# Kernel tuning notes

Measured on AMD Instinct MI355X. Metric: run time of the kernel, lower is better.

Reference implementation:

```python
import jax, jax.numpy as jnp
import numpy as np

N_NODES = 100000
N_EDGES = 1600000
N_GRAPHS = 2048
HID = 64
IN_F = 14
N_CLS = 2
EPS = 1e-5


def _gcn_conv(x, row, col, w_edge, W, b, n_nodes):
    # PyG GCNConv with add_self_loops=True, normalize=True.
    xw = x @ W  # [N, out]
    # degree on target nodes, self-loop contributes weight 1
    deg = jnp.zeros((n_nodes,), x.dtype).at[col].add(w_edge) + 1.0
    dinv = deg ** -0.5
    norm = dinv[row] * w_edge * dinv[col]  # [E]
    out = jnp.zeros_like(xw).at[col].add(norm[:, None] * xw[row])
    out = out + (dinv * dinv)[:, None] * xw  # self-loop term
    return out + b


def _bn_relu(x, gamma, beta):
    mean = jnp.mean(x, axis=0)
    var = jnp.var(x, axis=0)  # biased, as PyTorch BN training normalization
    y = gamma * (x - mean) * jax.lax.rsqrt(var + EPS) + beta
    return jax.nn.relu(y)


def setup_inputs() -> dict:
    key = jax.random.key(0)
    ks = jax.random.split(key, 8)
    x = jax.random.normal(ks[0], (N_NODES, IN_F), dtype=jnp.float32)
    edge_index = jax.random.randint(ks[1], (2, N_EDGES), 0, N_NODES, dtype=jnp.int64)
    batch = jnp.sort(jax.random.randint(ks[2], (N_NODES,), 0, N_GRAPHS, dtype=jnp.int64))
    edge_weight = jnp.ones((N_EDGES,), dtype=jnp.float32)
    def lin(k, fi, fo):
        s = 1.0 / np.sqrt(fi)
        kw, kb = jax.random.split(k)
        return (jax.random.uniform(kw, (fi, fo), jnp.float32, -s, s),
                jax.random.uniform(kb, (fo,), jnp.float32, -s, s))
    W1, b1 = lin(ks[3], IN_F, HID)
    W2, b2 = lin(ks[4], HID, HID)
    W3, b3 = lin(ks[5], HID, HID)
    fcW, fcb = lin(ks[6], HID, N_CLS)
    g = jnp.ones((HID,), jnp.float32)
    z = jnp.zeros((HID,), jnp.float32)
    return {
        "x": x, "edge_index": edge_index, "batch": batch, "edge_weight": edge_weight,
        "W1": W1, "b1": b1, "W2": W2, "b2": b2, "W3": W3, "b3": b3,
        "g1": g, "bt1": z, "g2": g, "bt2": z, "g3": g, "bt3": z,
        "fcW": fcW, "fcb": fcb,
    }


def reference(x, edge_index, batch, edge_weight, W1, b1, W2, b2, W3, b3,
              g1, bt1, g2, bt2, g3, bt3, fcW, fcb):
    row, col = edge_index[0], edge_index[1]
    n = x.shape[0]
    h = _bn_relu(_gcn_conv(x, row, col, edge_weight, W1, b1, n), g1, bt1)
    h = _bn_relu(_gcn_conv(h, row, col, edge_weight, W2, b2, n), g2, bt2)
    h = _bn_relu(_gcn_conv(h, row, col, edge_weight, W3, b3, n), g3, bt3)
    node_embs = h  # dropout p=0 is identity
    graph_emb = jax.ops.segment_sum(node_embs, batch, num_segments=N_GRAPHS)
    out = graph_emb @ fcW + fcb
    return (out, node_embs, graph_emb)
```

## Files before the change

kernel.cpp:

```cpp
#include <hip/hip_runtime.h>
#include <hip/hip_fp16.h>

#define N_NODES 100000
#define N_EDGES 1600000
#define EMAX2   1700000
#define N_GRAPHS 2048
#define HID 64
#define IN_F 14
#define N_CLS 2
#define EPS 1e-5f

#define BSHIFT 9
#define NBUCK 196
#define ABLOCKS 256
#define CHUNK (N_EDGES / ABLOCKS)

#define NBLK2 128
#define NCHUNK2 ((N_NODES + NBLK2 - 1) / NBLK2)

typedef _Float16 half_t;
typedef _Float16 half8 __attribute__((ext_vector_type(8)));
typedef float f32x4 __attribute__((ext_vector_type(4)));

#define GSTRIDE ((size_t)N_NODES * 16)


__global__ __launch_bounds__(256) void histA_kernel(const int* __restrict__ col,
                                                    int* __restrict__ histG) {
    __shared__ int hl[NBUCK];
    for (int i = threadIdx.x; i < NBUCK; i += 256) hl[i] = 0;
    __syncthreads();
    int e0 = blockIdx.x * CHUNK;
    for (int e = e0 + threadIdx.x; e < e0 + CHUNK; e += 256)
        atomicAdd(&hl[col[e] >> BSHIFT], 1);
    __syncthreads();
    for (int i = threadIdx.x; i < NBUCK; i += 256)
        histG[i * ABLOCKS + blockIdx.x] = hl[i];
}

__global__ __launch_bounds__(256) void scanS1_kernel(const int* __restrict__ histG,
                                                     int* __restrict__ bsumA) {
    __shared__ int ls[256];
    ls[threadIdx.x] = histG[blockIdx.x * 256 + threadIdx.x];
    __syncthreads();
    for (int off = 128; off > 0; off >>= 1) {
        if (threadIdx.x < off) ls[threadIdx.x] += ls[threadIdx.x + off];
        __syncthreads();
    }
    if (threadIdx.x == 0) bsumA[blockIdx.x] = ls[0];
}

__global__ __launch_bounds__(512) void topscan_kernel(int* __restrict__ bsum, int nb) {
    __shared__ int ls[512];
    int t = threadIdx.x;
    int v = (t < nb) ? bsum[t] : 0;
    ls[t] = v;
    __syncthreads();
    for (int off = 1; off < 512; off <<= 1) {
        int x = ls[t];
        if (t >= off) x += ls[t - off];
        __syncthreads();
        ls[t] = x;
        __syncthreads();
    }
    if (t < nb) bsum[t] = ls[t] - v;
}

__global__ __launch_bounds__(256) void scanS3_kernel(int* __restrict__ histG,
                                                     const int* __restrict__ bsumA,
                                                     int* __restrict__ ptr) {
    __shared__ int ls[256];
    int idx = blockIdx.x * 256 + threadIdx.x;
    int v = histG[idx];
    ls[threadIdx.x] = v;
    __syncthreads();
    for (int off = 1; off < 256; off <<= 1) {
        int x = ls[threadIdx.x];
        if (threadIdx.x >= off) x += ls[threadIdx.x - off];
        __syncthreads();
        ls[threadIdx.x] = x;
        __syncthreads();
    }
    histG[idx] = ls[threadIdx.x] - v + bsumA[blockIdx.x];
    if (blockIdx.x == 0 && threadIdx.x == 0) ptr[N_NODES] = N_EDGES;
}

__global__ __launch_bounds__(256) void scatterA_kernel(const int* __restrict__ row,
                                                       const int* __restrict__ col,
                                                       const float* __restrict__ w,
                                                       const int* __restrict__ histG,
                                                       int2* __restrict__ EA) {
    __shared__ int cur[NBUCK];
    for (int i = threadIdx.x; i < NBUCK; i += 256)
        cur[i] = histG[i * ABLOCKS + blockIdx.x];
    __syncthreads();
    int e0 = blockIdx.x * CHUNK;
    for (int e = e0 + threadIdx.x; e < e0 + CHUNK; e += 256) {
        int c = col[e];
        int r = row[e];
        int fx = (int)__float2uint_rn(w[e] * 8192.0f);
        int pos = atomicAdd(&cur[c >> BSHIFT], 1);
        EA[pos] = make_int2(r, (fx << 17) | c);
    }
}

__global__ __launch_bounds__(256) void bucketA_kernel(const int2* __restrict__ EA,
                                                      const int* __restrict__ bsumA,
                                                      int* __restrict__ ptr,
                                                      float* __restrict__ dinv) {
    __shared__ int hist[512], wsum[512];
    int b = blockIdx.x;
    int beg = bsumA[b];
    int end = (b == NBUCK - 1) ? N_EDGES : bsumA[b + 1];
    int i0 = threadIdx.x, i1 = threadIdx.x + 256;
    hist[i0] = 0; hist[i1] = 0;
    wsum[i0] = 0; wsum[i1] = 0;
    __syncthreads();
    for (int e = beg + threadIdx.x; e < end; e += 256) {
        int2 ed = EA[e];
        int c9 = ed.y & 511;
        atomicAdd(&hist[c9], 1);
        atomicAdd(&wsum[c9], (int)((unsigned int)ed.y >> 17));
    }
    __syncthreads();
    int cnt0 = hist[i0], cnt1 = hist[i1];
    for (int off = 1; off < 512; off <<= 1) {
        int v0 = hist[i0], v1 = hist[i1];
        int a0 = (i0 >= off) ? hist[i0 - off] : 0;
        int a1 = (i1 >= off) ? hist[i1 - off] : 0;
        __syncthreads();
        hist[i0] = v0 + a0;
        hist[i1] = v1 + a1;
        __syncthreads();
    }
    int excl0 = hist[i0] - cnt0, excl1 = hist[i1] - cnt1;
    int col0 = (b << BSHIFT) + i0, col1 = (b << BSHIFT) + i1;
    if (col0 < N_NODES) {
        ptr[col0] = beg + excl0;
        dinv[col0] = rsqrtf(1.0f + (float)wsum[i0] * (1.0f / 8192.0f));
    }
    if (col1 < N_NODES) {
        ptr[col1] = beg + excl1;
        dinv[col1] = rsqrtf(1.0f + (float)wsum[i1] * (1.0f / 8192.0f));
    }
}


__global__ __launch_bounds__(256) void histD_kernel(const int* __restrict__ ptr,
                                                    int* __restrict__ histD) {
    __shared__ int hl[2048];
    for (int i = threadIdx.x; i < 2048; i += 256) hl[i] = 0;
    __syncthreads();
    int n0 = blockIdx.x * NCHUNK2;
    int n1 = n0 + NCHUNK2; if (n1 > N_NODES) n1 = N_NODES;
    for (int n = n0 + threadIdx.x; n < n1; n += 256) {
        int d = ptr[n + 1] - ptr[n];
        if (d > 255) d = 255;
        atomicAdd(&hl[((threadIdx.x & 7) << 8) + d], 1);
    }
    __syncthreads();
    int s = 0;
#pragma unroll
    for (int c = 0; c < 8; c++) s += hl[(c << 8) + threadIdx.x];
    histD[threadIdx.x * NBLK2 + blockIdx.x] = s;
}

__global__ __launch_bounds__(128) void scanD1_kernel(const int* __restrict__ histD,
                                                     int* __restrict__ rowTot) {
    __shared__ int ls[128];
    ls[threadIdx.x] = histD[blockIdx.x * NBLK2 + threadIdx.x];
    __syncthreads();
    for (int off = 64; off > 0; off >>= 1) {
        if (threadIdx.x < off) ls[threadIdx.x] += ls[threadIdx.x + off];
        __syncthreads();
    }
    if (threadIdx.x == 0) rowTot[blockIdx.x] = ls[0];
}

__global__ __launch_bounds__(256) void topscanD_kernel(const int* __restrict__ rowTot,
                                                       int* __restrict__ nodeExcl,
                                                       int* __restrict__ edgeExcl,
                                                       int* __restrict__ ptrS) {
    __shared__ int a[256], b[256];
    int t = threadIdx.x;
    int cnt = rowTot[t];
    int dpad = (t + 1) & ~1;
    int ec = cnt * dpad;
    a[t] = cnt; b[t] = ec;
    __syncthreads();
    for (int off = 1; off < 256; off <<= 1) {
        int va = a[t], vb = b[t];
        if (t >= off) { va += a[t - off]; vb += b[t - off]; }
        __syncthreads();
        a[t] = va; b[t] = vb;
        __syncthreads();
    }
    nodeExcl[t] = a[t] - cnt;
    edgeExcl[t] = b[t] - ec;
    if (t == 255) ptrS[N_NODES] = b[255];
}

__global__ __launch_bounds__(128) void scanD3_kernel(int* __restrict__ histD,
                                                     const int* __restrict__ nodeExcl) {
    __shared__ int ls[128];
    int idx = blockIdx.x * NBLK2 + threadIdx.x;
    int v = histD[idx];
    ls[threadIdx.x] = v;
    __syncthreads();
    for (int off = 1; off < 128; off <<= 1) {
        int x = ls[threadIdx.x];
        if (threadIdx.x >= off) x += ls[threadIdx.x - off];
        __syncthreads();
        ls[threadIdx.x] = x;
        __syncthreads();
    }
    histD[idx] = ls[threadIdx.x] - v + nodeExcl[blockIdx.x];
}

__global__ __launch_bounds__(256) void scatterD_kernel(const int* __restrict__ ptr,
                                                       const int* __restrict__ histD,
                                                       const int* __restrict__ nodeExcl,
                                                       const int* __restrict__ edgeExcl,
                                                       int* __restrict__ perm,
                                                       int* __restrict__ ptrS,
                                                       int* __restrict__ newbase) {
    __shared__ int cur[256];
    cur[threadIdx.x] = histD[threadIdx.x * NBLK2 + blockIdx.x];
    __syncthreads();
    int n0 = blockIdx.x * NCHUNK2;
    int n1 = n0 + NCHUNK2; if (n1 > N_NODES) n1 = N_NODES;
    for (int n = n0 + threadIdx.x; n < n1; n += 256) {
        int d = ptr[n + 1] - ptr[n];
        if (d > 255) d = 255;
        int dpad = (d + 1) & ~1;
        int pos = atomicAdd(&cur[d], 1);
        int ebase = edgeExcl[d] + (pos - nodeExcl[d]) * dpad;
        perm[pos] = n;
        ptrS[pos] = ebase;
        newbase[n] = ebase;
    }
}

__global__ __launch_bounds__(256) void bucketB_kernel(const int2* __restrict__ EA,
                                                      const int* __restrict__ bsumA,
                                                      const int* __restrict__ newbase,
                                                      const float* __restrict__ dinv,
                                                      unsigned int* __restrict__ srcoff,
                                                      half_t* __restrict__ normh) {
    __shared__ int cur[512];
    int b = blockIdx.x;
    int beg = bsumA[b];
    int end = (b == NBUCK - 1) ? N_EDGES : bsumA[b + 1];
    int i0 = threadIdx.x, i1 = threadIdx.x + 256;
    int col0 = (b << BSHIFT) + i0, col1 = (b << BSHIFT) + i1;
    cur[i0] = (col0 < N_NODES) ? newbase[col0] : 0;
    cur[i1] = (col1 < N_NODES) ? newbase[col1] : 0;
    __syncthreads();
    for (int e = beg + threadIdx.x; e < end; e += 256) {
        int2 ed = EA[e];
        int c = ed.y & 0x1ffff;
        float w = (float)((unsigned int)ed.y >> 17) * (1.0f / 8192.0f);
        float nrm = dinv[ed.x] * w * dinv[c];
        int pos = atomicAdd(&cur[c & 511], 1);
        srcoff[pos] = (unsigned int)ed.x << 5;
        normh[pos] = (half_t)nrm;
    }
}


template <int K>
__global__ __launch_bounds__(256) void gemm_kernel(const float* __restrict__ h,
                                                   const float* __restrict__ W,
                                                   half_t* __restrict__ xw, int n_nodes) {
    int f = threadIdx.x & 63;
    float wcol[K];
#pragma unroll
    for (int k = 0; k < K; k++) wcol[k] = W[k * HID + f];
    half_t* xg = xw + (size_t)(f >> 4) * GSTRIDE + (f & 15);
    int wave = (blockIdx.x * blockDim.x + threadIdx.x) >> 6;
    int nwaves = (gridDim.x * blockDim.x) >> 6;
    for (int n = wave; n < n_nodes; n += nwaves) {
        const float* hr = h + (size_t)n * K;
        float acc = 0.f;
#pragma unroll
        for (int k = 0; k < K; k++) acc += hr[k] * wcol[k];
        xg[(size_t)n * 16] = (half_t)acc;
    }
}

__global__ __launch_bounds__(256) void gemm_bn_mfma_kernel(const half_t* __restrict__ h,
                                                           const float* __restrict__ W,
                                                           const float* __restrict__ stats,
                                                           const float* __restrict__ gamma,
                                                           const float* __restrict__ beta,
                                                           half_t* __restrict__ xw, int n_nodes) {
    __shared__ float sc_s[HID], sh_s[HID];
    if (threadIdx.x < 64) {
        float mean = stats[threadIdx.x] * (1.0f / N_NODES);
        float var = stats[64 + threadIdx.x] * (1.0f / N_NODES) - mean * mean;
        float sc = gamma[threadIdx.x] * rsqrtf(var + EPS);
        sc_s[threadIdx.x] = sc;
        sh_s[threadIdx.x] = beta[threadIdx.x] - mean * sc;
    }
    __syncthreads();
    int lane = threadIdx.x & 63;
    int col16 = lane & 15;
    int quad = lane >> 4;

    float scA[2][8], shA[2][8];
#pragma unroll
    for (int kh = 0; kh < 2; kh++)
#pragma unroll
        for (int j = 0; j < 8; j++) {
            int k = kh * 32 + quad * 8 + j;
            scA[kh][j] = sc_s[k];
            shA[kh][j] = sh_s[k];
        }

    half8 bfrag[4][2];
#pragma unroll
    for (int t = 0; t < 4; t++)
#pragma unroll
        for (int kh = 0; kh < 2; kh++)
#pragma unroll
            for (int j = 0; j < 8; j++) {
                int k = kh * 32 + quad * 8 + j;
                bfrag[t][kh][j] = (half_t)W[k * HID + t * 16 + col16];
            }

    int wave = (blockIdx.x * blockDim.x + threadIdx.x) >> 6;
    int nwaves = (gridDim.x * blockDim.x) >> 6;
    int ntiles = n_nodes >> 4;
    for (int tIdx = wave; tIdx < ntiles; tIdx += nwaves) {
        int n0 = tIdx << 4;
        half8 afrag[2];
#pragma unroll
        for (int kh = 0; kh < 2; kh++) {
            int k0 = kh * 32 + quad * 8;
            const half_t* hp = h + (size_t)(k0 >> 4) * GSTRIDE
                                 + (size_t)(n0 + col16) * 16 + (k0 & 15);
            half8 raw = *(const half8*)hp;
#pragma unroll
            for (int j = 0; j < 8; j++) {
                float v = (float)raw[j] * scA[kh][j] + shA[kh][j];
                afrag[kh][j] = (half_t)fmaxf(v, 0.f);
            }
        }
        f32x4 acc[4];
#pragma unroll
        for (int t = 0; t < 4; t++) {
            f32x4 z = {0.f, 0.f, 0.f, 0.f};
            acc[t] = __builtin_amdgcn_mfma_f32_16x16x32_f16(afrag[0], bfrag[t][0], z, 0, 0, 0);
            acc[t] = __builtin_amdgcn_mfma_f32_16x16x32_f16(afrag[1], bfrag[t][1], acc[t], 0, 0, 0);
        }
#pragma unroll
        for (int t = 0; t < 4; t++) {
            half_t* xg = xw + (size_t)t * GSTRIDE;
#pragma unroll
            for (int r = 0; r < 4; r++) {
                int rowi = n0 + quad * 4 + r;
                xg[(size_t)rowi * 16 + col16] = (half_t)acc[t][r];
            }
        }
    }
}

__global__ __launch_bounds__(256) void gather_stats_kernel(const int* __restrict__ ptrS,
                                                           const int* __restrict__ perm,
                                                           const unsigned int* __restrict__ srcoff,
                                                           const unsigned int* __restrict__ normu,
                                                           const half_t* __restrict__ xw,
                                                           const float* __restrict__ dinv,
                                                           const float* __restrict__ b,
                                                           half_t* __restrict__ hp,
                                                           float* __restrict__ stats,
                                                           int n_nodes) {
    int g = (blockIdx.x & 7) >> 1;
    int grank = ((blockIdx.x >> 3) << 1) | (blockIdx.x & 1);
    int lane16 = threadIdx.x & 15;
    int quadLocal = threadIdx.x >> 4;
    int quadId = grank * 16 + quadLocal;
    int nquads = (gridDim.x >> 2) * 16;

    const half_t* xg = xw + (size_t)g * GSTRIDE;
    const char* xgc = (const char*)xg;
    unsigned int loff = (unsigned int)(lane16 * 2);
    half_t* hpg = hp + (size_t)g * GSTRIDE;
    int f = g * 16 + lane16;
    float bf = b[f];
    int base = ((threadIdx.x & 63) >> 4) * 16;

    float s = 0.f, s2 = 0.f;
    for (int i = quadId; i < n_nodes; i += nquads) {
        int node = perm[i];
        int beg = ptrS[i];
        int c = ptrS[i + 1] - beg;
        __half2 acc0 = __float2half2_rn(0.f);
        __half2 acc1 = __float2half2_rn(0.f);
        for (int j0 = 0; j0 < c; j0 += 16) {
            int m = c - j0;
            if (m > 16) m = 16;
            int pairs = m >> 1;
            int ev = 0, nv = 0;
            if (lane16 < m) ev = (int)srcoff[beg + j0 + lane16];
            if (lane16 < pairs) nv = (int)normu[((beg + j0) >> 1) + lane16];
            int p = 0;
            for (; p + 2 <= pairs; p += 2) {
                unsigned int u0 = (unsigned int)__shfl(ev, base + 2 * p);
                unsigned int u1 = (unsigned int)__shfl(ev, base + 2 * p + 1);
                unsigned int u2 = (unsigned int)__shfl(ev, base + 2 * p + 2);
                unsigned int u3 = (unsigned int)__shfl(ev, base + 2 * p + 3);
                unsigned int nd0 = (unsigned int)__shfl(nv, base + p);
                unsigned int nd1 = (unsigned int)__shfl(nv, base + p + 1);
                __half h0 = *(const __half*)(xgc + (u0 + loff));
                __half h1 = *(const __half*)(xgc + (u1 + loff));
                __half h2 = *(const __half*)(xgc + (u2 + loff));
                __half h3 = *(const __half*)(xgc + (u3 + loff));
                __half2 n01 = *(__half2*)&nd0;
                __half2 n23 = *(__half2*)&nd1;
                acc0 = __hfma2(n01, __halves2half2(h0, h1), acc0);
                acc1 = __hfma2(n23, __halves2half2(h2, h3), acc1);
            }
            if (p < pairs) {
                unsigned int u0 = (unsigned int)__shfl(ev, base + 2 * p);
                unsigned int u1 = (unsigned int)__shfl(ev, base + 2 * p + 1);
                unsigned int nd0 = (unsigned int)__shfl(nv, base + p);
                __half h0 = *(const __half*)(xgc + (u0 + loff));
                __half h1 = *(const __half*)(xgc + (u1 + loff));
                __half2 n01 = *(__half2*)&nd0;
                acc0 = __hfma2(n01, __halves2half2(h0, h1), acc0);
            }
        }
        float accf = (__low2float(acc0) + __high2float(acc0))
                   + (__low2float(acc1) + __high2float(acc1));
        float di = dinv[node];
        float v = accf + di * di * (float)xg[(size_t)node * 16 + lane16] + bf;
        hpg[(size_t)node * 16 + lane16] = (half_t)v;
        s += v;
        s2 += v * v;
    }
    __shared__ float ls[256], ls2[256];
    ls[threadIdx.x] = s;
    ls2[threadIdx.x] = s2;
    __syncthreads();
    if (threadIdx.x < 16) {
        float a = 0.f, aa = 0.f;
#pragma unroll
        for (int k = 0; k < 16; k++) {
            a += ls[k * 16 + threadIdx.x];
            aa += ls2[k * 16 + threadIdx.x];
        }
        atomicAdd(&stats[g * 16 + threadIdx.x], a);
        atomicAdd(&stats[64 + g * 16 + threadIdx.x], aa);
    }
}

__global__ __launch_bounds__(256) void bn_relu_seg_kernel(const half_t* __restrict__ hpl,
                                                          float* __restrict__ h3,
                                                          const float* __restrict__ stats,
                                                          const float* __restrict__ gamma,
                                                          const float* __restrict__ beta,
                                                          const int* __restrict__ batch,
                                                          float* __restrict__ gemb,
                                                          int n_nodes) {
    int g = blockIdx.x * blockDim.x + threadIdx.x;
    int f = g & 63;
    int wave = g >> 6;
    int nwaves = (gridDim.x * blockDim.x) >> 6;
    int chunk = (n_nodes + nwaves - 1) / nwaves;
    int n0 = wave * chunk;
    int n1 = n0 + chunk;
    if (n1 > n_nodes) n1 = n_nodes;
    if (n0 >= n_nodes) return;
    float mean = stats[f] * (1.0f / N_NODES);
    float var = stats[64 + f] * (1.0f / N_NODES) - mean * mean;
    float sc = gamma[f] * rsqrtf(var + EPS);
    float sh = beta[f] - mean * sc;
    const half_t* hg = hpl + (size_t)(f >> 4) * GSTRIDE + (f & 15);
    int curg = batch[n0];
    float racc = 0.f;
    for (int n = n0; n < n1; n++) {
        int bg = batch[n];
        if (bg != curg) {
            atomicAdd(&gemb[(size_t)curg * HID + f], racc);
            racc = 0.f;
            curg = bg;
        }
        float v = (float)hg[(size_t)n * 16] * sc + sh;
        v = fmaxf(v, 0.f);
        h3[(size_t)n * HID + f] = v;
        racc += v;
    }
    atomicAdd(&gemb[(size_t)curg * HID + f], racc);
}

__global__ __launch_bounds__(256) void final_kernel(const float* __restrict__ gemb,
                                                    const float* __restrict__ fcW,
                                                    const float* __restrict__ fcb,
                                                    float* __restrict__ out) {
    int g = blockIdx.x * blockDim.x + threadIdx.x;
    if (g >= N_GRAPHS * N_CLS) return;
    int gr = g >> 1, c = g & 1;
    float acc = fcb[c];
#pragma unroll
    for (int k = 0; k < HID; k++) acc += gemb[gr * HID + k] * fcW[k * N_CLS + c];
    out[g] = acc;
}


extern "C" void kernel_launch(void* const* d_in, const int* in_sizes, int n_in,
                              void* d_out, int out_size, void* d_ws, size_t ws_size,
                              hipStream_t stream) {
    const float* x    = (const float*)d_in[0];
    const int*   ei   = (const int*)d_in[1];
    const int*   batch= (const int*)d_in[2];
    const float* ew   = (const float*)d_in[3];
    const float* W1   = (const float*)d_in[4];
    const float* b1   = (const float*)d_in[5];
    const float* W2   = (const float*)d_in[6];
    const float* b2   = (const float*)d_in[7];
    const float* W3   = (const float*)d_in[8];
    const float* b3   = (const float*)d_in[9];
    const float* g1   = (const float*)d_in[10];
    const float* bt1  = (const float*)d_in[11];
    const float* g2   = (const float*)d_in[12];
    const float* bt2  = (const float*)d_in[13];
    const float* g3   = (const float*)d_in[14];
    const float* bt3  = (const float*)d_in[15];
    const float* fcW  = (const float*)d_in[16];
    const float* fcb  = (const float*)d_in[17];

    const int* row = ei;
    const int* col = ei + N_EDGES;

    float* out_head  = (float*)d_out;
    float* node_embs = out_head + N_GRAPHS * N_CLS;
    float* gemb      = node_embs + (size_t)N_NODES * HID;

    char* bse = (char*)d_ws;
    half_t* xwh = (half_t*)bse;
    char* r1 = bse + (size_t)N_NODES * HID * 2;
    int2*   EA  = (int2*)r1;
    half_t* hpl = (half_t*)r1;
    char* r2 = r1 + (size_t)N_NODES * HID * 2;
    unsigned int* srcoff = (unsigned int*)r2;
    half_t* normh = (half_t*)(srcoff + EMAX2);
    char* r3 = r2 + (size_t)EMAX2 * 6;
    float* dinv  = (float*)r3;
    float* stats3 = dinv + N_NODES;
    int*   ptr   = (int*)(stats3 + 384);
    int*   histG = ptr + N_NODES + 1;
    int*   bsumA = histG + NBUCK * ABLOCKS;
    int*   histD = bsumA + NBUCK + 4;
    int*   rowTot = histD + 256 * NBLK2;
    int*   nodeExcl = rowTot + 256;
    int*   edgeExcl = nodeExcl + 256;
    int*   perm   = edgeExcl + 256;
    int*   newbase= perm + N_NODES;
    int*   ptrS   = newbase + N_NODES;

    const int B   = 256;
    const int gGS = 1024;
    const int gGA = 2048;

    hipMemsetAsync(srcoff, 0, (size_t)EMAX2 * 6, stream);
    hipMemsetAsync(stats3, 0, 384 * sizeof(float), stream);
    hipMemsetAsync(gemb, 0, (size_t)N_GRAPHS * HID * sizeof(float), stream);

    histA_kernel<<<ABLOCKS, B, 0, stream>>>(col, histG);
    scanS1_kernel<<<NBUCK, B, 0, stream>>>(histG, bsumA);
    topscan_kernel<<<1, 512, 0, stream>>>(bsumA, NBUCK);
    scanS3_kernel<<<NBUCK, B, 0, stream>>>(histG, bsumA, ptr);
    scatterA_kernel<<<ABLOCKS, B, 0, stream>>>(row, col, ew, histG, EA);
    bucketA_kernel<<<NBUCK, B, 0, stream>>>(EA, bsumA, ptr, dinv);

    histD_kernel<<<NBLK2, B, 0, stream>>>(ptr, histD);
    scanD1_kernel<<<256, 128, 0, stream>>>(histD, rowTot);
    topscanD_kernel<<<1, 256, 0, stream>>>(rowTot, nodeExcl, edgeExcl, ptrS);
    scanD3_kernel<<<256, 128, 0, stream>>>(histD, nodeExcl);
    scatterD_kernel<<<NBLK2, B, 0, stream>>>(ptr, histD, nodeExcl, edgeExcl,
                                             perm, ptrS, newbase);
    bucketB_kernel<<<NBUCK, B, 0, stream>>>(EA, bsumA, newbase, dinv, srcoff, normh);

    float* h3 = node_embs;

    gemm_kernel<IN_F><<<gGS, B, 0, stream>>>(x, W1, xwh, N_NODES);
    gather_stats_kernel<<<gGA, B, 0, stream>>>(ptrS, perm, srcoff,
                                               (const unsigned int*)normh, xwh,
                                               dinv, b1, hpl, stats3, N_NODES);

    gemm_bn_mfma_kernel<<<gGS, B, 0, stream>>>(hpl, W2, stats3, g1, bt1, xwh, N_NODES);
    gather_stats_kernel<<<gGA, B, 0, stream>>>(ptrS, perm, srcoff,
                                               (const unsigned int*)normh, xwh,
                                               dinv, b2, hpl, stats3 + 128, N_NODES);

    gemm_bn_mfma_kernel<<<gGS, B, 0, stream>>>(hpl, W3, stats3 + 128, g2, bt2, xwh, N_NODES);
    gather_stats_kernel<<<gGA, B, 0, stream>>>(ptrS, perm, srcoff,
                                               (const unsigned int*)normh, xwh,
                                               dinv, b3, hpl, stats3 + 256, N_NODES);

    bn_relu_seg_kernel<<<gGS, B, 0, stream>>>(hpl, h3, stats3 + 256, g3, bt3,
                                              batch, gemb, N_NODES);

    final_kernel<<<(N_GRAPHS * N_CLS + B - 1) / B, B, 0, stream>>>(gemb, fcW, fcb, out_head);
}
```

Before: 422.5 us.

## Assign one wave per node in gather, splitting edges across four lane groups

The gather kernel now gives each node a full 64-lane wave instead of a 16-lane quad. The four 16-lane groups each take a different edge in parallel, and their partial sums are combined with wave shuffles. Edge offsets and norms are loaded directly rather than broadcast by shuffle, and accumulation moves from packed half2 to fp32 FMA. The aim is more memory-level parallelism per node and fewer shuffles, at the cost of fewer nodes in flight per wave, idle lanes on odd tails, and a cross-group reduction.

```diff
diff --git a/kernel.cpp b/kernel.cpp
--- a/kernel.cpp
+++ b/kernel.cpp
@@ -368,7 +368,7 @@
 __global__ __launch_bounds__(256) void gather_stats_kernel(const int* __restrict__ ptrS,
                                                            const int* __restrict__ perm,
                                                            const unsigned int* __restrict__ srcoff,
-                                                           const unsigned int* __restrict__ normu,
+                                                           const half_t* __restrict__ normh,
                                                            const half_t* __restrict__ xw,
                                                            const float* __restrict__ dinv,
                                                            const float* __restrict__ b,
@@ -376,68 +376,64 @@
                                                            float* __restrict__ stats,
                                                            int n_nodes) {
     int g = (blockIdx.x & 7) >> 1;
-    int grank = ((blockIdx.x >> 3) << 1) | (blockIdx.x & 1);
-    int lane16 = threadIdx.x & 15;
-    int quadLocal = threadIdx.x >> 4;
-    int quadId = grank * 16 + quadLocal;
-    int nquads = (gridDim.x >> 2) * 16;
+    int wrank = ((((blockIdx.x >> 3) << 1) | (blockIdx.x & 1)) << 2) | (threadIdx.x >> 6);
+    int nwaves = gridDim.x;
+    int lane = threadIdx.x & 63;
+    int f = lane & 15;
+    int es = lane >> 4;
 
     const half_t* xg = xw + (size_t)g * GSTRIDE;
     const char* xgc = (const char*)xg;
-    unsigned int loff = (unsigned int)(lane16 * 2);
+    unsigned int loff = (unsigned int)(f * 2);
     half_t* hpg = hp + (size_t)g * GSTRIDE;
-    int f = g * 16 + lane16;
-    float bf = b[f];
-    int base = ((threadIdx.x & 63) >> 4) * 16;
+    float bf = b[g * 16 + f];
 
     float s = 0.f, s2 = 0.f;
-    for (int i = quadId; i < n_nodes; i += nquads) {
+    for (int i = wrank; i < n_nodes; i += nwaves) {
         int node = perm[i];
         int beg = ptrS[i];
         int c = ptrS[i + 1] - beg;
-        __half2 acc0 = __float2half2_rn(0.f);
-        __half2 acc1 = __float2half2_rn(0.f);
-        for (int j0 = 0; j0 < c; j0 += 16) {
-            int m = c - j0;
-            if (m > 16) m = 16;
-            int pairs = m >> 1;
-            int ev = 0, nv = 0;
-            if (lane16 < m) ev = (int)srcoff[beg + j0 + lane16];
-            if (lane16 < pairs) nv = (int)normu[((beg + j0) >> 1) + lane16];
-            int p = 0;
-            for (; p + 2 <= pairs; p += 2) {
-                unsigned int u0 = (unsigned int)__shfl(ev, base + 2 * p);
-                unsigned int u1 = (unsigned int)__shfl(ev, base + 2 * p + 1);
-                unsigned int u2 = (unsigned int)__shfl(ev, base + 2 * p + 2);
-                unsigned int u3 = (unsigned int)__shfl(ev, base + 2 * p + 3);
-                unsigned int nd0 = (unsigned int)__shfl(nv, base + p);
-                unsigned int nd1 = (unsigned int)__shfl(nv, base + p + 1);
-                __half h0 = *(const __half*)(xgc + (u0 + loff));
-                __half h1 = *(const __half*)(xgc + (u1 + loff));
-                __half h2 = *(const __half*)(xgc + (u2 + loff));
-                __half h3 = *(const __half*)(xgc + (u3 + loff));
-                __half2 n01 = *(__half2*)&nd0;
-                __half2 n23 = *(__half2*)&nd1;
-                acc0 = __hfma2(n01, __halves2half2(h0, h1), acc0);
-                acc1 = __hfma2(n23, __halves2half2(h2, h3), acc1);
+        const unsigned int* sop = srcoff + beg;
+        const half_t* nop = normh + beg;
+        float acc0 = 0.f, acc1 = 0.f;
+        int j0 = 0;
+        for (; j0 + 8 <= c; j0 += 8) {
+            unsigned int u0 = sop[j0 + es];
+            unsigned int u1 = sop[j0 + 4 + es];
+            float n0 = (float)nop[j0 + es];
+            float n1 = (float)nop[j0 + 4 + es];
+            float h0 = (float)*(const __half*)(xgc + (u0 + loff));
+            float h1 = (float)*(const __half*)(xgc + (u1 + loff));
+            acc0 = fmaf(n0, h0, acc0);
+            acc1 = fmaf(n1, h1, acc1);
+        }
+        if (j0 + 4 <= c) {
+            unsigned int u0 = sop[j0 + es];
+            float n0 = (float)nop[j0 + es];
+            float h0 = (float)*(const __half*)(xgc + (u0 + loff));
+            acc0 = fmaf(n0, h0, acc0);
+            j0 += 4;
+        }
+        if (j0 < c) {
+            unsigned int u0 = 0;
+            float n0 = 0.f;
+            if (es < 2) {
+                u0 = sop[j0 + es];
+                n0 = (float)nop[j0 + es];
             }
-            if (p < pairs) {
-                unsigned int u0 = (unsigned int)__shfl(ev, base + 2 * p);
-                unsigned int u1 = (unsigned int)__shfl(ev, base + 2 * p + 1);
-                unsigned int nd0 = (unsigned int)__shfl(nv, base + p);
-                __half h0 = *(const __half*)(xgc + (u0 + loff));
-                __half h1 = *(const __half*)(xgc + (u1 + loff));
-                __half2 n01 = *(__half2*)&nd0;
-                acc0 = __hfma2(n01, __halves2half2(h0, h1), acc0);
-            }
-        }
-        float accf = (__low2float(acc0) + __high2float(acc0))
-                   + (__low2float(acc1) + __high2float(acc1));
-        float di = dinv[node];
-        float v = accf + di * di * (float)xg[(size_t)node * 16 + lane16] + bf;
-        hpg[(size_t)node * 16 + lane16] = (half_t)v;
-        s += v;
-        s2 += v * v;
+            float h0 = (float)*(const __half*)(xgc + (u0 + loff));
+            acc0 = fmaf(n0, h0, acc0);
+        }
+        float acc = acc0 + acc1;
+        acc += __shfl_down(acc, 32);
+        acc += __shfl_down(acc, 16);
+        if (es == 0) {
+            float di = dinv[node];
+            float v = acc + di * di * (float)xg[(size_t)node * 16 + f] + bf;
+            hpg[(size_t)node * 16 + f] = (half_t)v;
+            s += v;
+            s2 += v * v;
+        }
     }
     __shared__ float ls[256], ls2[256];
     ls[threadIdx.x] = s;
@@ -585,18 +581,15 @@
     float* h3 = node_embs;
 
     gemm_kernel<IN_F><<<gGS, B, 0, stream>>>(x, W1, xwh, N_NODES);
-    gather_stats_kernel<<<gGA, B, 0, stream>>>(ptrS, perm, srcoff,
-                                               (const unsigned int*)normh, xwh,
+    gather_stats_kernel<<<gGA, B, 0, stream>>>(ptrS, perm, srcoff, normh, xwh,
                                                dinv, b1, hpl, stats3, N_NODES);
 
     gemm_bn_mfma_kernel<<<gGS, B, 0, stream>>>(hpl, W2, stats3, g1, bt1, xwh, N_NODES);
-    gather_stats_kernel<<<gGA, B, 0, stream>>>(ptrS, perm, srcoff,
-                                               (const unsigned int*)normh, xwh,
+    gather_stats_kernel<<<gGA, B, 0, stream>>>(ptrS, perm, srcoff, normh, xwh,
                                                dinv, b2, hpl, stats3 + 128, N_NODES);
 
     gemm_bn_mfma_kernel<<<gGS, B, 0, stream>>>(hpl, W3, stats3 + 128, g2, bt2, xwh, N_NODES);
-    gather_stats_kernel<<<gGA, B, 0, stream>>>(ptrS, perm, srcoff,
-                                               (const unsigned int*)normh, xwh,
+    gather_stats_kernel<<<gGA, B, 0, stream>>>(ptrS, perm, srcoff, normh, xwh,
                                                dinv, b3, hpl, stats3 + 256, N_NODES);
 
     bn_relu_seg_kernel<<<gGS, B, 0, stream>>>(hpl, h3, stats3 + 256, g3, bt3,
```

After: 633.5 us. 1.5x slower.

## Process node pairs per quad with software-prefetched edge metadata in aggregation

Applied to the files above, without the earlier changes.

The aggregation kernel now handles two degree-sorted nodes per 16-lane group per iteration, interleaving their gathers, and prefetches the next chunk's edge offsets/norms and the next pair's ptr/perm metadata ahead of use. Edge padding is raised from multiples of 2 to multiples of 4 (with a larger EMAX2 buffer) so the inner loop can always consume 4 edges without a tail branch. This aims to raise memory-level parallelism and hide latency of the dependent index loads, at the cost of more registers and extra padded zero-weight edges. It relies on n_nodes being even, since only npairs*2 nodes are processed.

```diff
diff --git a/kernel.cpp b/kernel.cpp
--- a/kernel.cpp
+++ b/kernel.cpp
@@ -3,7 +3,7 @@
 
 #define N_NODES 100000
 #define N_EDGES 1600000
-#define EMAX2   1700000
+#define EMAX2   2000000
 #define N_GRAPHS 2048
 #define HID 64
 #define IN_F 14
@@ -184,7 +184,7 @@
     __shared__ int a[256], b[256];
     int t = threadIdx.x;
     int cnt = rowTot[t];
-    int dpad = (t + 1) & ~1;
+    int dpad = (t + 3) & ~3;
     int ec = cnt * dpad;
     a[t] = cnt; b[t] = ec;
     __syncthreads();
@@ -232,7 +232,7 @@
     for (int n = n0 + threadIdx.x; n < n1; n += 256) {
         int d = ptr[n + 1] - ptr[n];
         if (d > 255) d = 255;
-        int dpad = (d + 1) & ~1;
+        int dpad = (d + 3) & ~3;
         int pos = atomicAdd(&cur[d], 1);
         int ebase = edgeExcl[d] + (pos - nodeExcl[d]) * dpad;
         perm[pos] = n;
@@ -391,53 +391,117 @@
     int base = ((threadIdx.x & 63) >> 4) * 16;
 
     float s = 0.f, s2 = 0.f;
-    for (int i = quadId; i < n_nodes; i += nquads) {
-        int node = perm[i];
-        int beg = ptrS[i];
-        int c = ptrS[i + 1] - beg;
-        __half2 acc0 = __float2half2_rn(0.f);
-        __half2 acc1 = __float2half2_rn(0.f);
-        for (int j0 = 0; j0 < c; j0 += 16) {
-            int m = c - j0;
-            if (m > 16) m = 16;
-            int pairs = m >> 1;
-            int ev = 0, nv = 0;
-            if (lane16 < m) ev = (int)srcoff[beg + j0 + lane16];
-            if (lane16 < pairs) nv = (int)normu[((beg + j0) >> 1) + lane16];
-            int p = 0;
-            for (; p + 2 <= pairs; p += 2) {
-                unsigned int u0 = (unsigned int)__shfl(ev, base + 2 * p);
-                unsigned int u1 = (unsigned int)__shfl(ev, base + 2 * p + 1);
-                unsigned int u2 = (unsigned int)__shfl(ev, base + 2 * p + 2);
-                unsigned int u3 = (unsigned int)__shfl(ev, base + 2 * p + 3);
-                unsigned int nd0 = (unsigned int)__shfl(nv, base + p);
-                unsigned int nd1 = (unsigned int)__shfl(nv, base + p + 1);
-                __half h0 = *(const __half*)(xgc + (u0 + loff));
-                __half h1 = *(const __half*)(xgc + (u1 + loff));
-                __half h2 = *(const __half*)(xgc + (u2 + loff));
-                __half h3 = *(const __half*)(xgc + (u3 + loff));
-                __half2 n01 = *(__half2*)&nd0;
-                __half2 n23 = *(__half2*)&nd1;
-                acc0 = __hfma2(n01, __halves2half2(h0, h1), acc0);
-                acc1 = __hfma2(n23, __halves2half2(h2, h3), acc1);
+
+    int npairs = n_nodes >> 1;
+    int idx = quadId;
+    int nodeA = 0, begA = 0, cA = 0, nodeB = 0, begB = 0, cB = 0;
+    int evA = 0, nvA = 0, evB = 0, nvB = 0;
+    if (idx < npairs) {
+        int iA = idx * 2;
+        nodeA = perm[iA];
+        nodeB = perm[iA + 1];
+        begA = ptrS[iA];
+        begB = ptrS[iA + 1];
+        cA = begB - begA;
+        cB = ptrS[iA + 2] - begB;
+        int mA = (cA > 16) ? 16 : cA;
+        int mB = (cB > 16) ? 16 : cB;
+        if (lane16 < mA) evA = (int)srcoff[begA + lane16];
+        if (lane16 < (mA >> 1)) nvA = (int)normu[(begA >> 1) + lane16];
+        if (lane16 < mB) evB = (int)srcoff[begB + lane16];
+        if (lane16 < (mB >> 1)) nvB = (int)normu[(begB >> 1) + lane16];
+    }
+
+    while (idx < npairs) {
+        int inext = idx + nquads;
+        int nodeA2 = 0, begA2 = 0, cA2 = 0, nodeB2 = 0, begB2 = 0, cB2 = 0;
+        if (inext < npairs) {
+            int iN = inext * 2;
+            nodeA2 = perm[iN];
+            nodeB2 = perm[iN + 1];
+            begA2 = ptrS[iN];
+            begB2 = ptrS[iN + 1];
+            cA2 = begB2 - begA2;
+            cB2 = ptrS[iN + 2] - begB2;
+        }
+        float selfA = (float)xg[(size_t)nodeA * 16 + lane16];
+        float diA = dinv[nodeA];
+        float selfB = (float)xg[(size_t)nodeB * 16 + lane16];
+        float diB = dinv[nodeB];
+
+        __half2 aA0 = __float2half2_rn(0.f), aA1 = __float2half2_rn(0.f);
+        __half2 aB0 = __float2half2_rn(0.f), aB1 = __float2half2_rn(0.f);
+
+        for (int j0 = 0; j0 < cB; j0 += 16) {
+            int mA = cA - j0; mA = (mA < 0) ? 0 : ((mA > 16) ? 16 : mA);
+            int mB = cB - j0; mB = (mB > 16) ? 16 : mB;
+            int pA = mA >> 1;
+            int pB = mB >> 1;
+            int evA2 = 0, nvA2 = 0, evB2 = 0, nvB2 = 0;
+            int j1 = j0 + 16;
+            if (j1 < cA) {
+                int m2 = cA - j1; if (m2 > 16) m2 = 16;
+                if (lane16 < m2) evA2 = (int)srcoff[begA + j1 + lane16];
+                if (lane16 < (m2 >> 1)) nvA2 = (int)normu[((begA + j1) >> 1) + lane16];
             }
-            if (p < pairs) {
-                unsigned int u0 = (unsigned int)__shfl(ev, base + 2 * p);
-                unsigned int u1 = (unsigned int)__shfl(ev, base + 2 * p + 1);
-                unsigned int nd0 = (unsigned int)__shfl(nv, base + p);
-                __half h0 = *(const __half*)(xgc + (u0 + loff));
-                __half h1 = *(const __half*)(xgc + (u1 + loff));
-                __half2 n01 = *(__half2*)&nd0;
-                acc0 = __hfma2(n01, __halves2half2(h0, h1), acc0);
+            if (j1 < cB) {
+                int m2 = cB - j1; if (m2 > 16) m2 = 16;
+                if (lane16 < m2) evB2 = (int)srcoff[begB + j1 + lane16];
+                if (lane16 < (m2 >> 1)) nvB2 = (int)normu[((begB + j1) >> 1) + lane16];
             }
-        }
-        float accf = (__low2float(acc0) + __high2float(acc0))
-                   + (__low2float(acc1) + __high2float(acc1));
-        float di = dinv[node];
-        float v = accf + di * di * (float)xg[(size_t)node * 16 + lane16] + bf;
-        hpg[(size_t)node * 16 + lane16] = (half_t)v;
-        s += v;
-        s2 += v * v;
+            for (int p = 0; p < pB; p += 2) {
+                unsigned int ub0 = (unsigned int)__shfl(evB, base + 2 * p);
+                unsigned int ub1 = (unsigned int)__shfl(evB, base + 2 * p + 1);
+                unsigned int ub2 = (unsigned int)__shfl(evB, base + 2 * p + 2);
+                unsigned int ub3 = (unsigned int)__shfl(evB, base + 2 * p + 3);
+                unsigned int nb0 = (unsigned int)__shfl(nvB, base + p);
+                unsigned int nb1 = (unsigned int)__shfl(nvB, base + p + 1);
+                __half hb0 = *(const __half*)(xgc + (ub0 + loff));
+                __half hb1 = *(const __half*)(xgc + (ub1 + loff));
+                __half hb2 = *(const __half*)(xgc + (ub2 + loff));
+                __half hb3 = *(const __half*)(xgc + (ub3 + loff));
+                aB0 = __hfma2(*(__half2*)&nb0, __halves2half2(hb0, hb1), aB0);
+                aB1 = __hfma2(*(__half2*)&nb1, __halves2half2(hb2, hb3), aB1);
+                if (p < pA) {
+                    unsigned int ua0 = (unsigned int)__shfl(evA, base + 2 * p);
+                    unsigned int ua1 = (unsigned int)__shfl(evA, base + 2 * p + 1);
+                    unsigned int ua2 = (unsigned int)__shfl(evA, base + 2 * p + 2);
+                    unsigned int ua3 = (unsigned int)__shfl(evA, base + 2 * p + 3);
+                    unsigned int na0 = (unsigned int)__shfl(nvA, base + p);
+                    unsigned int na1 = (unsigned int)__shfl(nvA, base + p + 1);
+                    __half ha0 = *(const __half*)(xgc + (ua0 + loff));
+                    __half ha1 = *(const __half*)(xgc + (ua1 + loff));
+                    __half ha2 = *(const __half*)(xgc + (ua2 + loff));
+                    __half ha3 = *(const __half*)(xgc + (ua3 + loff));
+                    aA0 = __hfma2(*(__half2*)&na0, __halves2half2(ha0, ha1), aA0);
+                    aA1 = __hfma2(*(__half2*)&na1, __halves2half2(ha2, ha3), aA1);
+                }
+            }
+            evA = evA2; nvA = nvA2; evB = evB2; nvB = nvB2;
+        }
+        if (inext < npairs) {
+            int mA0 = (cA2 > 16) ? 16 : cA2;
+            int mB0 = (cB2 > 16) ? 16 : cB2;
+            evA = (lane16 < mA0) ? (int)srcoff[begA2 + lane16] : 0;
+            nvA = (lane16 < (mA0 >> 1)) ? (int)normu[(begA2 >> 1) + lane16] : 0;
+            evB = (lane16 < mB0) ? (int)srcoff[begB2 + lane16] : 0;
+            nvB = (lane16 < (mB0 >> 1)) ? (int)normu[(begB2 >> 1) + lane16] : 0;
+        }
+
+        float accA = (__low2float(aA0) + __high2float(aA0))
+                   + (__low2float(aA1) + __high2float(aA1));
+        float vA = accA + diA * diA * selfA + bf;
+        hpg[(size_t)nodeA * 16 + lane16] = (half_t)vA;
+        float accB = (__low2float(aB0) + __high2float(aB0))
+                   + (__low2float(aB1) + __high2float(aB1));
+        float vB = accB + diB * diB * selfB + bf;
+        hpg[(size_t)nodeB * 16 + lane16] = (half_t)vB;
+        s += vA + vB;
+        s2 += vA * vA + vB * vB;
+
+        idx = inext;
+        nodeA = nodeA2; begA = begA2; cA = cA2;
+        nodeB = nodeB2; begB = begB2; cB = cB2;
     }
     __shared__ float ls[256], ls2[256];
     ls[threadIdx.x] = s;
```

Result: no change. 414.7 us (-1.9%).
